# Kernel optimization log

Hardware: AMD Instinct MI355X
Metric: run time of the kernel (lower is better)

The kernel has to match this reference:

```python
import jax, jax.numpy as jnp
import numpy as np

EPS = 1e-8  # torch CosineSimilarity default eps


def setup_inputs() -> dict:
    key = jax.random.key(0)
    k_emb, k_ei, k_w1, k_w2, k_b1, k_b2 = jax.random.split(key, 6)
    N, H, E = 50000, 256, 300000
    emb = jax.random.normal(k_emb, (N, H), dtype=jnp.float32)
    edge_index = jax.random.randint(k_ei, (2, E), 0, N, dtype=jnp.int64)
    # Xavier-uniform init for the two Linear layers (fan_in = fan_out = H)
    limit = float(np.sqrt(6.0 / (H + H)))
    W1 = jax.random.uniform(k_w1, (H, H), minval=-limit, maxval=limit, dtype=jnp.float32)
    W2 = jax.random.uniform(k_w2, (H, H), minval=-limit, maxval=limit, dtype=jnp.float32)
    b1 = jnp.zeros((H,), dtype=jnp.float32)
    b2 = jnp.zeros((H,), dtype=jnp.float32)
    return {"emb": emb, "edge_index": edge_index, "W1": W1, "b1": b1, "W2": W2, "b2": b2}


def _mlp(x, W1, b1, W2, b2):
    # Linear -> Dropout(eval: identity) -> ReLU -> Linear
    h = jax.nn.relu(x @ W1.T + b1)
    return h @ W2.T + b2


def _cosine(a, b):
    # torch.nn.CosineSimilarity(dim=1): dot / (max(||a||, eps) * max(||b||, eps))
    dot = jnp.sum(a * b, axis=1)
    na = jnp.maximum(jnp.linalg.norm(a, axis=1), EPS)
    nb = jnp.maximum(jnp.linalg.norm(b, axis=1), EPS)
    return dot / (na * nb)


def reference(emb, edge_index, W1, b1, W2, b2):
    col, row = edge_index[0], edge_index[1]
    f1 = emb[col]  # [E, H]
    f2 = emb[row]  # [E, H]
    g1 = _mlp(f1, W1, b1, W2, b2)
    g2 = _mlp(f2, W1, b1, W2, b2)
    return _cosine(g1, g2)  # [E] per-edge attention logits
```

## Files before the change

kernel.cpp:

```cpp
#include <hip/hip_runtime.h>
#include <stdint.h>

#define H 256
#define EPS 1e-8f

typedef __bf16 bf16x8 __attribute__((ext_vector_type(8)));
typedef float  f32x4  __attribute__((ext_vector_type(4)));

__device__ __forceinline__ unsigned short f2bf(float f) {
  unsigned u = __builtin_bit_cast(unsigned, f);
  u += 0x7FFFu + ((u >> 16) & 1u);
  return (unsigned short)(u >> 16);
}
__device__ __forceinline__ float bflo(unsigned u){ return __builtin_bit_cast(float, u << 16); }
__device__ __forceinline__ float bfhi(unsigned u){ return __builtin_bit_cast(float, u & 0xFFFF0000u); }

__device__ __forceinline__ void g2l16(const void* g, void* l) {
  __builtin_amdgcn_global_load_lds((__attribute__((address_space(1))) void*)g,
                                   (__attribute__((address_space(3))) void*)l, 16, 0, 0);
}

__global__ __launch_bounds__(256) void conv_w_kernel(
    const float* __restrict__ W1, const float* __restrict__ W2,
    unsigned short* __restrict__ w1B, unsigned short* __restrict__ w2B) {
  int i = (blockIdx.x * 256 + threadIdx.x) * 4;
  const int HH = H * H;
  if (i >= 2 * HH) return;
  const float* s = (i < HH) ? W1 : W2;
  unsigned short* d = (i < HH) ? w1B : w2B;
  int j = (i < HH) ? i : i - HH;
  float4 v = *(const float4*)(s + j);
  ushort4 o;
  o.x = f2bf(v.x); o.y = f2bf(v.y); o.z = f2bf(v.z); o.w = f2bf(v.w);
  *(ushort4*)(d + j) = o;
}

__global__ __launch_bounds__(256) void fused_mlp_kernel(
    const float* __restrict__ Af,
    const unsigned short* __restrict__ W1,
    const unsigned short* __restrict__ W2,
    const float* __restrict__ b1, const float* __restrict__ b2,
    unsigned short* __restrict__ G,
    float* __restrict__ rn, int N) {
  __shared__ unsigned short sA[2][64 * 32];
  __shared__ unsigned short sW[2][256 * 32];
  __shared__ unsigned short sH[64 * 256];
  __shared__ float ssb[64][2];

  const int tid  = threadIdx.x;
  const int wave = tid >> 6, lane = tid & 63;
  const int quad = lane >> 4, l16 = lane & 15;
  const int wr = wave >> 1, wn = wave & 1;
  const size_t bm = blockIdx.x;

  const int arow = tid >> 2, kch = (tid & 3) * 8;
  const int grow = (int)bm * 64 + arow;
  const bool avalid = grow < N;
  const int crow = avalid ? grow : (N - 1);
  const float* gAf = Af + (size_t)crow * H + kch;
  const unsigned short* gW1 = W1 + (size_t)arow * H + kch;
  const unsigned short* gW2 = W2 + (size_t)arow * H + kch;

  const float4 z4 = make_float4(0.f, 0.f, 0.f, 0.f);
  float4 ra[2][2];
#define LOAD_A(kt, slot)                                                        \
  do {                                                                          \
    ra[slot][0] = *(const float4*)(gAf + (kt) * 32);                            \
    ra[slot][1] = *(const float4*)(gAf + (kt) * 32 + 4);                        \
  } while (0)
#define WRITE_A(buf, slot)                                                      \
  do {                                                                          \
    float4 t0 = avalid ? ra[slot][0] : z4;                                      \
    float4 t1 = avalid ? ra[slot][1] : z4;                                      \
    uint4 p;                                                                    \
    p.x = (unsigned)f2bf(t0.x) | ((unsigned)f2bf(t0.y) << 16);                  \
    p.y = (unsigned)f2bf(t0.z) | ((unsigned)f2bf(t0.w) << 16);                  \
    p.z = (unsigned)f2bf(t1.x) | ((unsigned)f2bf(t1.y) << 16);                  \
    p.w = (unsigned)f2bf(t1.z) | ((unsigned)f2bf(t1.w) << 16);                  \
    *(uint4*)(&sA[buf][tid * 8]) = p;                                           \
  } while (0)
#define STAGE_W(gW, kt, buf)                                                    \
  do {                                                                          \
    _Pragma("unroll")                                                           \
    for (int c = 0; c < 4; c++)                                                 \
      g2l16((gW) + (size_t)(c * 64) * H + (kt) * 32, &sW[buf][c * 2048 + tid * 8]); \
  } while (0)

  f32x4 acc[8][2];
#pragma unroll
  for (int i = 0; i < 8; i++)
#pragma unroll
    for (int j = 0; j < 2; j++) acc[i][j] = (f32x4){0.f, 0.f, 0.f, 0.f};

  STAGE_W(gW1, 0, 0);
  LOAD_A(0, 0);
  LOAD_A(1, 1);
  WRITE_A(0, 0);
  asm volatile("s_waitcnt vmcnt(2) lgkmcnt(0)" ::: "memory");
  __builtin_amdgcn_s_barrier();

#pragma unroll
  for (int kt = 0; kt < 8; ++kt) {
    if (kt < 7) STAGE_W(gW1, kt + 1, (kt + 1) & 1);
    else        STAGE_W(gW2, 0, 0);
    if (kt < 6) LOAD_A(kt + 2, kt & 1);

    bf16x8 wf[8], af0, af1;
#pragma unroll
    for (int i = 0; i < 8; i++)
      wf[i] = *(const bf16x8*)(&sW[kt & 1][(wn * 128 + i * 16 + l16) * 32 + quad * 8]);
    af0 = *(const bf16x8*)(&sA[kt & 1][(wr * 32 + 0 * 16 + l16) * 32 + quad * 8]);
    af1 = *(const bf16x8*)(&sA[kt & 1][(wr * 32 + 1 * 16 + l16) * 32 + quad * 8]);

    if (kt < 7) WRITE_A((kt + 1) & 1, (kt + 1) & 1);

#pragma unroll
    for (int i = 0; i < 8; i++) {
      acc[i][0] = __builtin_amdgcn_mfma_f32_16x16x32_bf16(wf[i], af0, acc[i][0], 0, 0, 0);
      acc[i][1] = __builtin_amdgcn_mfma_f32_16x16x32_bf16(wf[i], af1, acc[i][1], 0, 0, 0);
    }

    if (kt < 7) {
      if (kt < 6) asm volatile("s_waitcnt vmcnt(2) lgkmcnt(0)" ::: "memory");
      else        asm volatile("s_waitcnt vmcnt(0) lgkmcnt(0)" ::: "memory");
      __builtin_amdgcn_s_barrier();
    }
  }

#pragma unroll
  for (int i = 0; i < 8; i++) {
    const int hcol = wn * 128 + i * 16 + quad * 4;
    const float4 bv = *(const float4*)(b1 + hcol);
#pragma unroll
    for (int j = 0; j < 2; j++) {
      const int row = wr * 32 + j * 16 + l16;
      f32x4 v = acc[i][j];
      unsigned short h0 = f2bf(fmaxf(v[0] + bv.x, 0.f));
      unsigned short h1 = f2bf(fmaxf(v[1] + bv.y, 0.f));
      unsigned short h2 = f2bf(fmaxf(v[2] + bv.z, 0.f));
      unsigned short h3 = f2bf(fmaxf(v[3] + bv.w, 0.f));
      uint2 p;
      p.x = (unsigned)h0 | ((unsigned)h1 << 16);
      p.y = (unsigned)h2 | ((unsigned)h3 << 16);
      unsigned off = (unsigned)(row * 512 + hcol * 2) ^ ((unsigned)(row & 7) << 4);
      *(uint2*)((char*)sH + off) = p;
    }
  }

  __syncthreads();

  f32x4 acc2[2][8];
#pragma unroll
  for (int i = 0; i < 2; i++)
#pragma unroll
    for (int j = 0; j < 8; j++) acc2[i][j] = (f32x4){0.f, 0.f, 0.f, 0.f};

#pragma unroll
  for (int kt = 0; kt < 8; ++kt) {
    if (kt < 7) STAGE_W(gW2, kt + 1, (kt + 1) & 1);

    bf16x8 wf2[8], hf[2];
#pragma unroll
    for (int j = 0; j < 8; j++)
      wf2[j] = *(const bf16x8*)(&sW[kt & 1][(wn * 128 + j * 16 + l16) * 32 + quad * 8]);
#pragma unroll
    for (int i = 0; i < 2; i++) {
      const int hrow = wr * 32 + i * 16 + l16;
      unsigned off = (unsigned)(hrow * 512 + kt * 64 + quad * 16) ^ ((unsigned)(hrow & 7) << 4);
      hf[i] = *(const bf16x8*)((const char*)sH + off);
    }
#pragma unroll
    for (int i = 0; i < 2; i++)
#pragma unroll
      for (int j = 0; j < 8; j++)
        acc2[i][j] = __builtin_amdgcn_mfma_f32_16x16x32_bf16(hf[i], wf2[j], acc2[i][j], 0, 0, 0);
    if (kt < 7) __syncthreads();
  }

  float b2v[8];
#pragma unroll
  for (int j = 0; j < 8; j++) b2v[j] = b2[wn * 128 + j * 16 + l16];
#pragma unroll
  for (int i = 0; i < 2; i++)
#pragma unroll
    for (int j = 0; j < 8; j++)
#pragma unroll
      for (int r = 0; r < 4; r++) acc2[i][j][r] += b2v[j];

  float ss[2][4];
#pragma unroll
  for (int i = 0; i < 2; i++)
#pragma unroll
    for (int r = 0; r < 4; r++) {
      float s = 0.f;
#pragma unroll
      for (int j = 0; j < 8; j++) s += acc2[i][j][r] * acc2[i][j][r];
      ss[i][r] = s;
    }
#pragma unroll
  for (int m = 1; m < 16; m <<= 1)
#pragma unroll
    for (int i = 0; i < 2; i++)
#pragma unroll
      for (int r = 0; r < 4; r++) ss[i][r] += __shfl_xor(ss[i][r], m, 64);
  if (l16 == 0) {
#pragma unroll
    for (int i = 0; i < 2; i++)
#pragma unroll
      for (int r = 0; r < 4; r++) ssb[wr * 32 + i * 16 + quad * 4 + r][wn] = ss[i][r];
  }
  __syncthreads();
  if (tid < 64) {
    float s2 = ssb[tid][0] + ssb[tid][1];
    rn[bm * 64 + tid] = 1.f / fmaxf(sqrtf(s2), EPS);
  }

#pragma unroll
  for (int i = 0; i < 2; i++)
#pragma unroll
    for (int j = 0; j < 8; j++) {
      const int gcol = wn * 128 + j * 16 + l16;
#pragma unroll
      for (int r = 0; r < 4; r++) {
        const size_t grow2 = bm * 64 + wr * 32 + i * 16 + quad * 4 + r;
        G[grow2 * H + gcol] = f2bf(acc2[i][j][r]);
      }
    }
#undef LOAD_A
#undef WRITE_A
#undef STAGE_W
}

__device__ __forceinline__ float dot_u4(uint4 a, uint4 b) {
  float s;
  s  = bflo(a.x) * bflo(b.x) + bfhi(a.x) * bfhi(b.x);
  s += bflo(a.y) * bflo(b.y) + bfhi(a.y) * bfhi(b.y);
  s += bflo(a.z) * bflo(b.z) + bfhi(a.z) * bfhi(b.z);
  s += bflo(a.w) * bflo(b.w) + bfhi(a.w) * bfhi(b.w);
  return s;
}

__global__ __launch_bounds__(256) void edge_cos_kernel(
    const int* __restrict__ ei, const unsigned short* __restrict__ g,
    const float* __restrict__ rn, float* __restrict__ out, int E) {
  const int lane = threadIdx.x & 63;
  const int wid  = threadIdx.x >> 6;
  const int l8   = lane & 7;
  const int sub  = lane >> 3;
  const int e    = blockIdx.x * 32 + wid * 8 + sub;
  if (e >= E) return;
  const int c = ei[e], r = ei[E + e];
  const uint4* gc = (const uint4*)(g + (size_t)c * H);
  const uint4* gr = (const uint4*)(g + (size_t)r * H);
  uint4 a0 = gc[l8], a1 = gc[l8 + 8], a2 = gc[l8 + 16], a3 = gc[l8 + 24];
  uint4 b0 = gr[l8], b1 = gr[l8 + 8], b2 = gr[l8 + 16], b3 = gr[l8 + 24];
  float d = dot_u4(a0, b0) + dot_u4(a1, b1) + dot_u4(a2, b2) + dot_u4(a3, b3);
  d += __shfl_xor(d, 4, 8);
  d += __shfl_xor(d, 2, 8);
  d += __shfl_xor(d, 1, 8);
  if (l8 == 0) out[e] = d * rn[c] * rn[r];
}

extern "C" void kernel_launch(void* const* d_in, const int* in_sizes, int n_in,
                              void* d_out, int out_size, void* d_ws, size_t ws_size,
                              hipStream_t stream) {
  const float* emb = (const float*)d_in[0];
  const int*   ei  = (const int*)d_in[1];
  const float* W1  = (const float*)d_in[2];
  const float* b1  = (const float*)d_in[3];
  const float* W2  = (const float*)d_in[4];
  const float* b2  = (const float*)d_in[5];
  float* out = (float*)d_out;

  const int NH = in_sizes[0];
  const int N  = NH / H;
  const int E  = in_sizes[1] / 2;
  const int Mp = ((N + 63) / 64) * 64;

  char* ws = (char*)d_ws;
  unsigned short* gB   = (unsigned short*)ws; ws += (size_t)Mp * H * 2;
  unsigned short* w1B  = (unsigned short*)ws; ws += (size_t)H * H * 2;
  unsigned short* w2B  = (unsigned short*)ws; ws += (size_t)H * H * 2;
  float* rn            = (float*)ws;

  conv_w_kernel<<<(2 * H * H / 4 + 255) / 256, 256, 0, stream>>>(W1, W2, w1B, w2B);

  fused_mlp_kernel<<<Mp / 64, 256, 0, stream>>>(emb, w1B, w2B, b1, b2, gB, rn, N);

  edge_cos_kernel<<<(E + 31) / 32, 256, 0, stream>>>(ei, gB, rn, out, E);
}
```

Before: 158.2 us.

## Stage weight tiles through registers with deeper prefetch instead of direct global-to-LDS loads

Replaces the direct global_load_lds weight staging with register-staged loads that are written to LDS by threads. Weights are now prefetched two K-tiles ahead and activations three tiles ahead. Barriers now wait only on LDS counters, so global loads can stay in flight across iterations instead of being drained with vmcnt waits. The cost is more VGPRs for the in-flight buffers and extra LDS write instructions, which may reduce occupancy or add issue pressure.

```diff
diff --git a/kernel.cpp b/kernel.cpp
--- a/kernel.cpp
+++ b/kernel.cpp
@@ -14,11 +14,6 @@
 }
 __device__ __forceinline__ float bflo(unsigned u){ return __builtin_bit_cast(float, u << 16); }
 __device__ __forceinline__ float bfhi(unsigned u){ return __builtin_bit_cast(float, u & 0xFFFF0000u); }
-
-__device__ __forceinline__ void g2l16(const void* g, void* l) {
-  __builtin_amdgcn_global_load_lds((__attribute__((address_space(1))) void*)g,
-                                   (__attribute__((address_space(3))) void*)l, 16, 0, 0);
-}
 
 __global__ __launch_bounds__(256) void conv_w_kernel(
     const float* __restrict__ W1, const float* __restrict__ W2,
@@ -62,16 +57,18 @@
   const unsigned short* gW2 = W2 + (size_t)arow * H + kch;
 
   const float4 z4 = make_float4(0.f, 0.f, 0.f, 0.f);
-  float4 ra[2][2];
-#define LOAD_A(kt, slot)                                                        \
-  do {                                                                          \
-    ra[slot][0] = *(const float4*)(gAf + (kt) * 32);                            \
-    ra[slot][1] = *(const float4*)(gAf + (kt) * 32 + 4);                        \
-  } while (0)
-#define WRITE_A(buf, slot)                                                      \
-  do {                                                                          \
-    float4 t0 = avalid ? ra[slot][0] : z4;                                      \
-    float4 t1 = avalid ? ra[slot][1] : z4;                                      \
+  float4 rf[3][2];
+  uint4  rw[2][4];
+
+#define LOADA(kt, s)                                                            \
+  do {                                                                          \
+    rf[s][0] = *(const float4*)(gAf + (kt) * 32);                               \
+    rf[s][1] = *(const float4*)(gAf + (kt) * 32 + 4);                           \
+  } while (0)
+#define WRITEA(s, buf)                                                          \
+  do {                                                                          \
+    float4 t0 = avalid ? rf[s][0] : z4;                                         \
+    float4 t1 = avalid ? rf[s][1] : z4;                                         \
     uint4 p;                                                                    \
     p.x = (unsigned)f2bf(t0.x) | ((unsigned)f2bf(t0.y) << 16);                  \
     p.y = (unsigned)f2bf(t0.z) | ((unsigned)f2bf(t0.w) << 16);                  \
@@ -79,11 +76,22 @@
     p.w = (unsigned)f2bf(t1.z) | ((unsigned)f2bf(t1.w) << 16);                  \
     *(uint4*)(&sA[buf][tid * 8]) = p;                                           \
   } while (0)
-#define STAGE_W(gW, kt, buf)                                                    \
+#define LOADW(gW, kt, s)                                                        \
   do {                                                                          \
     _Pragma("unroll")                                                           \
     for (int c = 0; c < 4; c++)                                                 \
-      g2l16((gW) + (size_t)(c * 64) * H + (kt) * 32, &sW[buf][c * 2048 + tid * 8]); \
+      rw[s][c] = *(const uint4*)((gW) + (size_t)(c * 64) * H + (kt) * 32);      \
+  } while (0)
+#define WRITEW(s, buf)                                                          \
+  do {                                                                          \
+    _Pragma("unroll")                                                           \
+    for (int c = 0; c < 4; c++)                                                 \
+      *(uint4*)(&sW[buf][c * 2048 + tid * 8]) = rw[s][c];                       \
+  } while (0)
+#define LGKM_BAR()                                                              \
+  do {                                                                          \
+    asm volatile("s_waitcnt lgkmcnt(0)" ::: "memory");                          \
+    __builtin_amdgcn_s_barrier();                                               \
   } while (0)
 
   f32x4 acc[8][2];
@@ -92,18 +100,20 @@
 #pragma unroll
     for (int j = 0; j < 2; j++) acc[i][j] = (f32x4){0.f, 0.f, 0.f, 0.f};
 
-  STAGE_W(gW1, 0, 0);
-  LOAD_A(0, 0);
-  LOAD_A(1, 1);
-  WRITE_A(0, 0);
-  asm volatile("s_waitcnt vmcnt(2) lgkmcnt(0)" ::: "memory");
-  __builtin_amdgcn_s_barrier();
+  LOADW(gW1, 0, 0);
+  LOADW(gW1, 1, 1);
+  LOADA(0, 0); LOADA(1, 1); LOADA(2, 2);
+  WRITEW(0, 0);
+  WRITEA(0, 0);
+  LGKM_BAR();
 
 #pragma unroll
   for (int kt = 0; kt < 8; ++kt) {
-    if (kt < 7) STAGE_W(gW1, kt + 1, (kt + 1) & 1);
-    else        STAGE_W(gW2, 0, 0);
-    if (kt < 6) LOAD_A(kt + 2, kt & 1);
+    if (kt) LGKM_BAR();
+    if (kt < 6) LOADW(gW1, kt + 2, kt & 1);
+    if (kt == 6) LOADW(gW2, 0, 0);
+    if (kt == 7) LOADW(gW2, 1, 1);
+    if (kt < 5) LOADA(kt + 3, kt % 3);
 
     bf16x8 wf[8], af0, af1;
 #pragma unroll
@@ -112,18 +122,17 @@
     af0 = *(const bf16x8*)(&sA[kt & 1][(wr * 32 + 0 * 16 + l16) * 32 + quad * 8]);
     af1 = *(const bf16x8*)(&sA[kt & 1][(wr * 32 + 1 * 16 + l16) * 32 + quad * 8]);
 
-    if (kt < 7) WRITE_A((kt + 1) & 1, (kt + 1) & 1);
+    if (kt < 7) {
+      WRITEW((kt + 1) & 1, (kt + 1) & 1);
+      WRITEA((kt + 1) % 3, (kt + 1) & 1);
+    } else {
+      WRITEW(0, 0);
+    }
 
 #pragma unroll
     for (int i = 0; i < 8; i++) {
       acc[i][0] = __builtin_amdgcn_mfma_f32_16x16x32_bf16(wf[i], af0, acc[i][0], 0, 0, 0);
       acc[i][1] = __builtin_amdgcn_mfma_f32_16x16x32_bf16(wf[i], af1, acc[i][1], 0, 0, 0);
-    }
-
-    if (kt < 7) {
-      if (kt < 6) asm volatile("s_waitcnt vmcnt(2) lgkmcnt(0)" ::: "memory");
-      else        asm volatile("s_waitcnt vmcnt(0) lgkmcnt(0)" ::: "memory");
-      __builtin_amdgcn_s_barrier();
     }
   }
 
@@ -147,7 +156,7 @@
     }
   }
 
-  __syncthreads();
+  LGKM_BAR();
 
   f32x4 acc2[2][8];
 #pragma unroll
@@ -157,7 +166,8 @@
 
 #pragma unroll
   for (int kt = 0; kt < 8; ++kt) {
-    if (kt < 7) STAGE_W(gW2, kt + 1, (kt + 1) & 1);
+    if (kt) LGKM_BAR();
+    if (kt < 6) LOADW(gW2, kt + 2, kt & 1);
 
     bf16x8 wf2[8], hf[2];
 #pragma unroll
@@ -169,12 +179,14 @@
       unsigned off = (unsigned)(hrow * 512 + kt * 64 + quad * 16) ^ ((unsigned)(hrow & 7) << 4);
       hf[i] = *(const bf16x8*)((const char*)sH + off);
     }
+
+    if (kt < 7) WRITEW((kt + 1) & 1, (kt + 1) & 1);
+
 #pragma unroll
     for (int i = 0; i < 2; i++)
 #pragma unroll
       for (int j = 0; j < 8; j++)
         acc2[i][j] = __builtin_amdgcn_mfma_f32_16x16x32_bf16(hf[i], wf2[j], acc2[i][j], 0, 0, 0);
-    if (kt < 7) __syncthreads();
   }
 
   float b2v[8];
@@ -226,9 +238,11 @@
         G[grow2 * H + gcol] = f2bf(acc2[i][j][r]);
       }
     }
-#undef LOAD_A
-#undef WRITE_A
-#undef STAGE_W
+#undef LOADA
+#undef WRITEA
+#undef LOADW
+#undef WRITEW
+#undef LGKM_BAR
 }
 
 __device__ __forceinline__ float dot_u4(uint4 a, uint4 b) {
```

Result: slower. 170.1 us (+7.5%).

## Drop double-buffered staging in fused MLP to raise occupancy

Applied to the files above, without the earlier changes.

Replaces the double-buffered A and W shared-memory staging with single buffers and a simple load, sync, compute, sync loop. It also adds a minimum-blocks hint of 4 to launch bounds. Halving the staging LDS and dropping the prefetch registers is meant to fit more workgroups per CU, so other blocks hide latency instead of in-block software pipelining. The cost is lost overlap of global loads with MFMA inside each block and an extra barrier per k-step.

```diff
diff --git a/kernel.cpp b/kernel.cpp
--- a/kernel.cpp
+++ b/kernel.cpp
@@ -35,15 +35,15 @@
   *(ushort4*)(d + j) = o;
 }
 
-__global__ __launch_bounds__(256) void fused_mlp_kernel(
+__global__ __launch_bounds__(256, 4) void fused_mlp_kernel(
     const float* __restrict__ Af,
     const unsigned short* __restrict__ W1,
     const unsigned short* __restrict__ W2,
     const float* __restrict__ b1, const float* __restrict__ b2,
     unsigned short* __restrict__ G,
     float* __restrict__ rn, int N) {
-  __shared__ unsigned short sA[2][64 * 32];
-  __shared__ unsigned short sW[2][256 * 32];
+  __shared__ unsigned short sA[64 * 32];
+  __shared__ unsigned short sW[256 * 32];
   __shared__ unsigned short sH[64 * 256];
   __shared__ float ssb[64][2];
 
@@ -60,30 +60,25 @@
   const float* gAf = Af + (size_t)crow * H + kch;
   const unsigned short* gW1 = W1 + (size_t)arow * H + kch;
   const unsigned short* gW2 = W2 + (size_t)arow * H + kch;
-
   const float4 z4 = make_float4(0.f, 0.f, 0.f, 0.f);
-  float4 ra[2][2];
-#define LOAD_A(kt, slot)                                                        \
+
+#define STAGE_A(kt)                                                             \
   do {                                                                          \
-    ra[slot][0] = *(const float4*)(gAf + (kt) * 32);                            \
-    ra[slot][1] = *(const float4*)(gAf + (kt) * 32 + 4);                        \
+    float4 a0 = *(const float4*)(gAf + (kt) * 32);                              \
+    float4 a1 = *(const float4*)(gAf + (kt) * 32 + 4);                          \
+    if (!avalid) { a0 = z4; a1 = z4; }                                          \
+    uint4 p;                                                                    \
+    p.x = (unsigned)f2bf(a0.x) | ((unsigned)f2bf(a0.y) << 16);                  \
+    p.y = (unsigned)f2bf(a0.z) | ((unsigned)f2bf(a0.w) << 16);                  \
+    p.z = (unsigned)f2bf(a1.x) | ((unsigned)f2bf(a1.y) << 16);                  \
+    p.w = (unsigned)f2bf(a1.z) | ((unsigned)f2bf(a1.w) << 16);                  \
+    *(uint4*)(&sA[tid * 8]) = p;                                                \
   } while (0)
-#define WRITE_A(buf, slot)                                                      \
-  do {                                                                          \
-    float4 t0 = avalid ? ra[slot][0] : z4;                                      \
-    float4 t1 = avalid ? ra[slot][1] : z4;                                      \
-    uint4 p;                                                                    \
-    p.x = (unsigned)f2bf(t0.x) | ((unsigned)f2bf(t0.y) << 16);                  \
-    p.y = (unsigned)f2bf(t0.z) | ((unsigned)f2bf(t0.w) << 16);                  \
-    p.z = (unsigned)f2bf(t1.x) | ((unsigned)f2bf(t1.y) << 16);                  \
-    p.w = (unsigned)f2bf(t1.z) | ((unsigned)f2bf(t1.w) << 16);                  \
-    *(uint4*)(&sA[buf][tid * 8]) = p;                                           \
-  } while (0)
-#define STAGE_W(gW, kt, buf)                                                    \
+#define STAGE_W(gW, kt)                                                         \
   do {                                                                          \
     _Pragma("unroll")                                                           \
     for (int c = 0; c < 4; c++)                                                 \
-      g2l16((gW) + (size_t)(c * 64) * H + (kt) * 32, &sW[buf][c * 2048 + tid * 8]); \
+      g2l16((gW) + (size_t)(c * 64) * H + (kt) * 32, &sW[c * 2048 + tid * 8]);  \
   } while (0)
 
   f32x4 acc[8][2];
@@ -92,38 +87,24 @@
 #pragma unroll
     for (int j = 0; j < 2; j++) acc[i][j] = (f32x4){0.f, 0.f, 0.f, 0.f};
 
-  STAGE_W(gW1, 0, 0);
-  LOAD_A(0, 0);
-  LOAD_A(1, 1);
-  WRITE_A(0, 0);
-  asm volatile("s_waitcnt vmcnt(2) lgkmcnt(0)" ::: "memory");
-  __builtin_amdgcn_s_barrier();
-
 #pragma unroll
   for (int kt = 0; kt < 8; ++kt) {
-    if (kt < 7) STAGE_W(gW1, kt + 1, (kt + 1) & 1);
-    else        STAGE_W(gW2, 0, 0);
-    if (kt < 6) LOAD_A(kt + 2, kt & 1);
+    if (kt) __syncthreads();
+    STAGE_A(kt);
+    STAGE_W(gW1, kt);
+    __syncthreads();
 
     bf16x8 wf[8], af0, af1;
 #pragma unroll
     for (int i = 0; i < 8; i++)
-      wf[i] = *(const bf16x8*)(&sW[kt & 1][(wn * 128 + i * 16 + l16) * 32 + quad * 8]);
-    af0 = *(const bf16x8*)(&sA[kt & 1][(wr * 32 + 0 * 16 + l16) * 32 + quad * 8]);
-    af1 = *(const bf16x8*)(&sA[kt & 1][(wr * 32 + 1 * 16 + l16) * 32 + quad * 8]);
-
-    if (kt < 7) WRITE_A((kt + 1) & 1, (kt + 1) & 1);
+      wf[i] = *(const bf16x8*)(&sW[(wn * 128 + i * 16 + l16) * 32 + quad * 8]);
+    af0 = *(const bf16x8*)(&sA[(wr * 32 + 0 * 16 + l16) * 32 + quad * 8]);
+    af1 = *(const bf16x8*)(&sA[(wr * 32 + 1 * 16 + l16) * 32 + quad * 8]);
 
 #pragma unroll
     for (int i = 0; i < 8; i++) {
       acc[i][0] = __builtin_amdgcn_mfma_f32_16x16x32_bf16(wf[i], af0, acc[i][0], 0, 0, 0);
       acc[i][1] = __builtin_amdgcn_mfma_f32_16x16x32_bf16(wf[i], af1, acc[i][1], 0, 0, 0);
-    }
-
-    if (kt < 7) {
-      if (kt < 6) asm volatile("s_waitcnt vmcnt(2) lgkmcnt(0)" ::: "memory");
-      else        asm volatile("s_waitcnt vmcnt(0) lgkmcnt(0)" ::: "memory");
-      __builtin_amdgcn_s_barrier();
     }
   }
 
@@ -157,12 +138,14 @@
 
 #pragma unroll
   for (int kt = 0; kt < 8; ++kt) {
-    if (kt < 7) STAGE_W(gW2, kt + 1, (kt + 1) & 1);
+    if (kt) __syncthreads();
+    STAGE_W(gW2, kt);
+    __syncthreads();
 
     bf16x8 wf2[8], hf[2];
 #pragma unroll
     for (int j = 0; j < 8; j++)
-      wf2[j] = *(const bf16x8*)(&sW[kt & 1][(wn * 128 + j * 16 + l16) * 32 + quad * 8]);
+      wf2[j] = *(const bf16x8*)(&sW[(wn * 128 + j * 16 + l16) * 32 + quad * 8]);
 #pragma unroll
     for (int i = 0; i < 2; i++) {
       const int hrow = wr * 32 + i * 16 + l16;
@@ -174,7 +157,6 @@
 #pragma unroll
       for (int j = 0; j < 8; j++)
         acc2[i][j] = __builtin_amdgcn_mfma_f32_16x16x32_bf16(hf[i], wf2[j], acc2[i][j], 0, 0, 0);
-    if (kt < 7) __syncthreads();
   }
 
   float b2v[8];
@@ -226,8 +208,7 @@
         G[grow2 * H + gcol] = f2bf(acc2[i][j][r]);
       }
     }
-#undef LOAD_A
-#undef WRITE_A
+#undef STAGE_A
 #undef STAGE_W
 }
 
```

Measured after the change: 157.5 us. No clear change (-0.4%).
